# Performance work log

Hardware: AMD Instinct MI355X
Metric: run time of the kernel (lower is better)

Reference implementation:

```python
import jax, jax.numpy as jnp
import numpy as np

IN_CAP_N = 1152   # 128*3*3
IN_CAP_SZ = 5
OUT_CAP_N = 55
OUT_CAP_SZ = 1
BATCH = 8192
ROUTING_ITERS = 2


def setup_inputs() -> dict:
    key = jax.random.key(0)
    k_u, k_w = jax.random.split(key)
    u = jax.random.normal(k_u, (BATCH, IN_CAP_SZ, 128, 3, 3), dtype=jnp.float32)
    W = jax.random.normal(k_w, (1, IN_CAP_N, OUT_CAP_SZ), dtype=jnp.float32)
    b = jnp.zeros((OUT_CAP_N, OUT_CAP_SZ), dtype=jnp.float32)
    return {"u": u, "W": W, "b": b}


def _squash(s):
    # s: (B, 55, 1)
    norm_sq = jnp.sum(s * s, axis=2, keepdims=True)
    norm = jnp.sqrt(norm_sq)
    return norm / (1.0 + norm_sq) * s


def reference(u, W, b):
    B = u.shape[0]
    u_ = u.reshape(B, IN_CAP_SZ, IN_CAP_N)              # (B, 5, 1152)
    u_hat = jnp.matmul(u_, jnp.broadcast_to(W, (B, IN_CAP_N, OUT_CAP_SZ)))  # (B, 5, 1)
    # routing logits, expanded from (55,1) param to (B, 55, 5)
    b_ij = jnp.broadcast_to(b, (B, OUT_CAP_N, IN_CAP_SZ))
    v = None
    for _ in range(ROUTING_ITERS):
        c = jax.nn.softmax(b_ij, axis=1)                 # softmax over out-capsules
        s = jnp.matmul(c, u_hat)                         # (B, 55, 5)@(B, 5, 1) -> (B, 55, 1)
        v = _squash(s)
        b_ij = b_ij + jnp.matmul(v, jnp.swapaxes(u_hat, 1, 2))  # (B, 55, 5)
    return v
```

## Files before the change

### kernel.cpp

```cpp
#include <hip/hip_runtime.h>
#include <math.h>

#define IN_CAP_N   1152
#define ROW_F2     576
#define IN_CAP_SZ  5
#define OUT_CAP_N  55
#define NBATCH     8192
#define WAVES_PER_BLOCK 4

typedef float f32x2 __attribute__((ext_vector_type(2)));

__global__ __launch_bounds__(256) void digitcaps_fused(
    const float* __restrict__ u,
    const float* __restrict__ W,
    const float* __restrict__ bparam,
    float* __restrict__ out)
{
    const int lane = threadIdx.x & 63;
    const int wave = threadIdx.x >> 6;
    const int b    = blockIdx.x * WAVES_PER_BLOCK + wave;

    const f32x2* W2 = (const f32x2*)W;
    f32x2 wreg[9];
    #pragma unroll
    for (int p = 0; p < 9; ++p) wreg[p] = W2[p * 64 + lane];

    const f32x2* u2 = (const f32x2*)(u + (size_t)b * (IN_CAP_SZ * IN_CAP_N));
    f32x2 uv[IN_CAP_SZ][9];
    #pragma unroll
    for (int i = 0; i < IN_CAP_SZ; ++i) {
        const f32x2* row = u2 + i * ROW_F2;
        #pragma unroll
        for (int p = 0; p < 9; ++p)
            uv[i][p] = __builtin_nontemporal_load(&row[p * 64 + lane]);
    }

    float h[IN_CAP_SZ];
    #pragma unroll
    for (int i = 0; i < IN_CAP_SZ; ++i) {
        float a0 = 0.f, a1 = 0.f;
        #pragma unroll
        for (int p = 0; p < 9; ++p) {
            a0 += uv[i][p].x * wreg[p].x;
            a1 += uv[i][p].y * wreg[p].y;
        }
        h[i] = a0 + a1;
    }
    #pragma unroll
    for (int off = 32; off > 0; off >>= 1) {
        #pragma unroll
        for (int i = 0; i < IN_CAP_SZ; ++i)
            h[i] += __shfl_xor(h[i], off, 64);
    }

    const bool active = (lane < OUT_CAP_N);
    const float b0 = active ? bparam[lane] : -INFINITY;

    float m = b0;
    #pragma unroll
    for (int off = 32; off > 0; off >>= 1)
        m = fmaxf(m, __shfl_xor(m, off, 64));
    float e = active ? __expf(b0 - m) : 0.f;
    float sum = e;
    #pragma unroll
    for (int off = 32; off > 0; off >>= 1)
        sum += __shfl_xor(sum, off, 64);
    const float c1 = e / sum;
    const float hs = h[0] + h[1] + h[2] + h[3] + h[4];
    float s = c1 * hs;
    float v = fabsf(s) * s / (1.f + s * s);

    float x[IN_CAP_SZ], mm[IN_CAP_SZ], ee[IN_CAP_SZ], ss[IN_CAP_SZ];
    #pragma unroll
    for (int i = 0; i < IN_CAP_SZ; ++i) { x[i] = b0 + v * h[i]; mm[i] = x[i]; }
    #pragma unroll
    for (int off = 32; off > 0; off >>= 1) {
        #pragma unroll
        for (int i = 0; i < IN_CAP_SZ; ++i)
            mm[i] = fmaxf(mm[i], __shfl_xor(mm[i], off, 64));
    }
    #pragma unroll
    for (int i = 0; i < IN_CAP_SZ; ++i)
        ee[i] = active ? __expf(x[i] - mm[i]) : 0.f;
    #pragma unroll
    for (int i = 0; i < IN_CAP_SZ; ++i) ss[i] = ee[i];
    #pragma unroll
    for (int off = 32; off > 0; off >>= 1) {
        #pragma unroll
        for (int i = 0; i < IN_CAP_SZ; ++i)
            ss[i] += __shfl_xor(ss[i], off, 64);
    }
    s = 0.f;
    #pragma unroll
    for (int i = 0; i < IN_CAP_SZ; ++i) s += (ee[i] / ss[i]) * h[i];
    v = fabsf(s) * s / (1.f + s * s);

    if (active)
        __builtin_nontemporal_store(v, &out[(size_t)b * OUT_CAP_N + lane]);
}

extern "C" void kernel_launch(void* const* d_in, const int* in_sizes, int n_in,
                              void* d_out, int out_size, void* d_ws, size_t ws_size,
                              hipStream_t stream) {
    const float* u  = (const float*)d_in[0];
    const float* W  = (const float*)d_in[1];
    const float* bp = (const float*)d_in[2];
    float* out = (float*)d_out;
    digitcaps_fused<<<NBATCH / WAVES_PER_BLOCK, WAVES_PER_BLOCK * 64, 0, stream>>>(u, W, bp, out);
}
```

Measured before the change: 245.1 us.

## Process two batches per wave with 16-byte vector loads

Result: no change. 242.2 us (-1.2%).

```diff
diff --git a/kernel.cpp b/kernel.cpp
--- a/kernel.cpp
+++ b/kernel.cpp
@@ -1,14 +1,14 @@
 #include <hip/hip_runtime.h>
 #include <math.h>
 
-#define IN_CAP_N   1152
-#define ROW_F2     576
 #define IN_CAP_SZ  5
 #define OUT_CAP_N  55
 #define NBATCH     8192
+#define ROW_F4     288
+#define PAIR_F4    2880
 #define WAVES_PER_BLOCK 4
 
-typedef float f32x2 __attribute__((ext_vector_type(2)));
+typedef float f32x4 __attribute__((ext_vector_type(4)));
 
 __global__ __launch_bounds__(256) void digitcaps_fused(
     const float* __restrict__ u,
@@ -16,46 +16,51 @@
     const float* __restrict__ bparam,
     float* __restrict__ out)
 {
-    const int lane = threadIdx.x & 63;
-    const int wave = threadIdx.x >> 6;
-    const int b    = blockIdx.x * WAVES_PER_BLOCK + wave;
+    const int lane  = threadIdx.x & 63;
+    const int wave  = threadIdx.x >> 6;
+    const int bpair = blockIdx.x * WAVES_PER_BLOCK + wave;
+    const int bA    = bpair * 2;
 
-    const f32x2* W2 = (const f32x2*)W;
-    f32x2 wreg[9];
+    const f32x4* W4 = (const f32x4*)W;
+    f32x4 wreg[9];
+    wreg[0] = W4[lane];
+    wreg[1] = W4[64 + lane];
+    wreg[2] = W4[128 + lane];
+    wreg[3] = W4[192 + lane];
+    wreg[4] = (lane < 32) ? W4[256 + lane] : W4[lane - 32];
+    wreg[5] = W4[32 + lane];
+    wreg[6] = W4[96 + lane];
+    wreg[7] = W4[160 + lane];
+    wreg[8] = W4[224 + lane];
+
+    const f32x4* u4 = (const f32x4*)u + (size_t)bpair * PAIR_F4;
+    float acc[2 * IN_CAP_SZ];
     #pragma unroll
-    for (int p = 0; p < 9; ++p) wreg[p] = W2[p * 64 + lane];
+    for (int r = 0; r < 10; ++r) acc[r] = 0.f;
 
-    const f32x2* u2 = (const f32x2*)(u + (size_t)b * (IN_CAP_SZ * IN_CAP_N));
-    f32x2 uv[IN_CAP_SZ][9];
     #pragma unroll
-    for (int i = 0; i < IN_CAP_SZ; ++i) {
-        const f32x2* row = u2 + i * ROW_F2;
-        #pragma unroll
-        for (int p = 0; p < 9; ++p)
-            uv[i][p] = __builtin_nontemporal_load(&row[p * 64 + lane]);
+    for (int p = 0; p < 45; ++p) {
+        f32x4 v4 = __builtin_nontemporal_load(&u4[p * 64 + lane]);
+        f32x4 w4 = wreg[p % 9];
+        float g = v4.x * w4.x + v4.y * w4.y + v4.z * w4.z + v4.w * w4.w;
+        const int r0 = (p * 64) / ROW_F4;
+        const int r1 = (p * 64 + 63) / ROW_F4;
+        if (r0 == r1) {
+            acc[r0] += g;
+        } else {
+            if (lane < 32) acc[r0] += g; else acc[r1] += g;
+        }
     }
 
-    float h[IN_CAP_SZ];
-    #pragma unroll
-    for (int i = 0; i < IN_CAP_SZ; ++i) {
-        float a0 = 0.f, a1 = 0.f;
-        #pragma unroll
-        for (int p = 0; p < 9; ++p) {
-            a0 += uv[i][p].x * wreg[p].x;
-            a1 += uv[i][p].y * wreg[p].y;
-        }
-        h[i] = a0 + a1;
-    }
     #pragma unroll
     for (int off = 32; off > 0; off >>= 1) {
         #pragma unroll
-        for (int i = 0; i < IN_CAP_SZ; ++i)
-            h[i] += __shfl_xor(h[i], off, 64);
+        for (int r = 0; r < 10; ++r)
+            acc[r] += __shfl_xor(acc[r], off, 64);
     }
 
     const bool active = (lane < OUT_CAP_N);
     const float b0 = active ? bparam[lane] : -INFINITY;
-
     float m = b0;
     #pragma unroll
     for (int off = 32; off > 0; off >>= 1)
@@ -66,37 +71,45 @@
     for (int off = 32; off > 0; off >>= 1)
         sum += __shfl_xor(sum, off, 64);
     const float c1 = e / sum;
-    const float hs = h[0] + h[1] + h[2] + h[3] + h[4];
-    float s = c1 * hs;
-    float v = fabsf(s) * s / (1.f + s * s);
 
-    float x[IN_CAP_SZ], mm[IN_CAP_SZ], ee[IN_CAP_SZ], ss[IN_CAP_SZ];
+    float vout[2];
     #pragma unroll
-    for (int i = 0; i < IN_CAP_SZ; ++i) { x[i] = b0 + v * h[i]; mm[i] = x[i]; }
-    #pragma unroll
-    for (int off = 32; off > 0; off >>= 1) {
+    for (int t = 0; t < 2; ++t) {
+        const float* h = acc + IN_CAP_SZ * t;
+        const float hs = h[0] + h[1] + h[2] + h[3] + h[4];
+        float s = c1 * hs;
+        float v = fabsf(s) * s / (1.f + s * s);
+
+        float x[IN_CAP_SZ], mm[IN_CAP_SZ], ee[IN_CAP_SZ], ss[IN_CAP_SZ];
+        #pragma unroll
+        for (int i = 0; i < IN_CAP_SZ; ++i) { x[i] = b0 + v * h[i]; mm[i] = x[i]; }
+        #pragma unroll
+        for (int off = 32; off > 0; off >>= 1) {
+            #pragma unroll
+            for (int i = 0; i < IN_CAP_SZ; ++i)
+                mm[i] = fmaxf(mm[i], __shfl_xor(mm[i], off, 64));
+        }
         #pragma unroll
         for (int i = 0; i < IN_CAP_SZ; ++i)
-            mm[i] = fmaxf(mm[i], __shfl_xor(mm[i], off, 64));
+            ee[i] = active ? __expf(x[i] - mm[i]) : 0.f;
+        #pragma unroll
+        for (int i = 0; i < IN_CAP_SZ; ++i) ss[i] = ee[i];
+        #pragma unroll
+        for (int off = 32; off > 0; off >>= 1) {
+            #pragma unroll
+            for (int i = 0; i < IN_CAP_SZ; ++i)
+                ss[i] += __shfl_xor(ss[i], off, 64);
+        }
+        s = 0.f;
+        #pragma unroll
+        for (int i = 0; i < IN_CAP_SZ; ++i) s += (ee[i] / ss[i]) * h[i];
+        vout[t] = fabsf(s) * s / (1.f + s * s);
     }
-    #pragma unroll
-    for (int i = 0; i < IN_CAP_SZ; ++i)
-        ee[i] = active ? __expf(x[i] - mm[i]) : 0.f;
-    #pragma unroll
-    for (int i = 0; i < IN_CAP_SZ; ++i) ss[i] = ee[i];
-    #pragma unroll
-    for (int off = 32; off > 0; off >>= 1) {
-        #pragma unroll
-        for (int i = 0; i < IN_CAP_SZ; ++i)
-            ss[i] += __shfl_xor(ss[i], off, 64);
+
+    if (active) {
+        __builtin_nontemporal_store(vout[0], &out[(size_t)bA * OUT_CAP_N + lane]);
+        __builtin_nontemporal_store(vout[1], &out[(size_t)(bA + 1) * OUT_CAP_N + lane]);
     }
-    s = 0.f;
-    #pragma unroll
-    for (int i = 0; i < IN_CAP_SZ; ++i) s += (ee[i] / ss[i]) * h[i];
-    v = fabsf(s) * s / (1.f + s * s);
-
-    if (active)
-        __builtin_nontemporal_store(v, &out[(size_t)b * OUT_CAP_N + lane]);
 }
 
 extern "C" void kernel_launch(void* const* d_in, const int* in_sizes, int n_in,
@@ -106,5 +119,5 @@
     const float* W  = (const float*)d_in[1];
     const float* bp = (const float*)d_in[2];
     float* out = (float*)d_out;
-    digitcaps_fused<<<NBATCH / WAVES_PER_BLOCK, WAVES_PER_BLOCK * 64, 0, stream>>>(u, W, bp, out);
+    digitcaps_fused<<<NBATCH / 2 / WAVES_PER_BLOCK, WAVES_PER_BLOCK * 64, 0, stream>>>(u, W, bp, out);
 }
```
